# Kernel tuning notes

Measured on AMD Instinct MI355X. Metric: run time of the kernel, lower is better.

## Reference

```python
import jax, jax.numpy as jnp
import numpy as np

TEMP = 10.0  # softmax_ called with N=10.0 in reduce_func

def qmul(a, b):
    # Hamilton product, rows are (w, x, y, z)
    aw, ax, ay, az = a[..., 0], a[..., 1], a[..., 2], a[..., 3]
    bw, bx, by, bz = b[..., 0], b[..., 1], b[..., 2], b[..., 3]
    return jnp.stack([
        aw * bw - ax * bx - ay * by - az * bz,
        aw * bx + ax * bw + ay * bz - az * by,
        aw * by - ax * bz + ay * bw + az * bx,
        aw * bz + ax * by - ay * bx + az * bw,
    ], axis=-1)

def setup_inputs() -> dict:
    key = jax.random.key(0)
    k1, k2, k3, k4, k5, k6 = jax.random.split(key, 6)
    N, E = 100000, 3200000
    node_levels = jax.random.uniform(k1, (N,), dtype=jnp.float32)
    node_q = jax.random.normal(k2, (N, 4), dtype=jnp.float32)
    node_q = node_q / jnp.linalg.norm(node_q, axis=1, keepdims=True)
    edge_rel_q = jax.random.normal(k3, (E, 4), dtype=jnp.float32)
    edge_rel_q = edge_rel_q / jnp.linalg.norm(edge_rel_q, axis=1, keepdims=True)
    edge_w = jax.random.uniform(k4, (E,), dtype=jnp.float32)
    src = jax.random.randint(k5, (E,), 0, N, dtype=jnp.int32)
    dst = jax.random.randint(k6, (E,), 0, N, dtype=jnp.int32)
    return {"node_levels": node_levels, "node_q": node_q,
            "edge_rel_q": edge_rel_q, "edge_w": edge_w,
            "src": src, "dst": dst}

def reference(node_levels, node_q, edge_rel_q, edge_w, src, dst):
    N = node_q.shape[0]
    # per-edge message: accumulated quaternion rel_q * q_src
    accu_q = qmul(edge_rel_q, node_q[src])          # [E,4]
    l_src = node_levels[src]                        # [E]
    # softmax logits: cost = w * l (self term has w = 1)
    cost_e = TEMP * edge_w * l_src                  # [E]
    cost_self = TEMP * node_levels                  # [N]
    # segmented stable softmax over {self} U in-edges per dst node
    seg_max = jax.ops.segment_max(cost_e, dst, num_segments=N)
    m = jnp.maximum(seg_max, cost_self)             # [N]
    exp_e = jnp.exp(cost_e - m[dst])                # [E]
    exp_self = jnp.exp(cost_self - m)               # [N]
    Z = jax.ops.segment_sum(exp_e, dst, num_segments=N) + exp_self
    # weighted sums
    sum_q = jax.ops.segment_sum(exp_e[:, None] * accu_q, dst, num_segments=N) \
            + exp_self[:, None] * node_q            # [N,4]
    sum_l = jax.ops.segment_sum(exp_e * l_src, dst, num_segments=N) \
            + exp_self * node_levels                # [N]
    out_q = sum_q / Z[:, None]
    out_levels = sum_l / Z
    # F.normalize(q, p=2, dim=1) with eps=1e-12 clamp
    norm = jnp.maximum(jnp.linalg.norm(out_q, axis=1, keepdims=True), 1e-12)
    return out_q / norm, out_levels
```

## Files before the change

### kernel.cpp

```cpp
#include <hip/hip_runtime.h>
#include <hip/hip_fp16.h>

#define TEMP 10.0f
#define TPB 512
#define HTPB 256
#define NBLK 1024
#define SHIFT 9
#define GSZ 512
#define BMAX 256
#define TILE 1568
#define GTPB 1024
#define GT 4096

typedef float v2f  __attribute__((ext_vector_type(2)));
typedef float vf4  __attribute__((ext_vector_type(4)));
typedef unsigned uv4 __attribute__((ext_vector_type(4)));

__device__ __forceinline__ int   nt_i (const int* p)   { return __builtin_nontemporal_load(p); }
__device__ __forceinline__ float nt_f (const float* p) { return __builtin_nontemporal_load(p); }
__device__ __forceinline__ float4 nt_f4(const float4* p) {
    vf4 v = __builtin_nontemporal_load((const vf4*)p);
    return make_float4(v.x, v.y, v.z, v.w);
}
__device__ __forceinline__ uint4 nt_u4(const uint4* p) {
    uv4 v = __builtin_nontemporal_load((const uv4*)p);
    uint4 r; r.x = v.x; r.y = v.y; r.z = v.z; r.w = v.w; return r;
}

__device__ __forceinline__ void pk_fadd(float* p, float a, float b) {
#if __has_builtin(__builtin_amdgcn_global_atomic_fadd_v2f32)
    v2f v; v.x = a; v.y = b;
    __builtin_amdgcn_global_atomic_fadd_v2f32(
        (__attribute__((address_space(1))) v2f*)p, v);
#else
    atomicAdd(p, a); atomicAdd(p + 1, b);
#endif
}

__device__ __forceinline__ void hamilton(float4 a, float4 b,
                                         float& ow, float& ox, float& oy, float& oz) {
    ow = a.x*b.x - a.y*b.y - a.z*b.z - a.w*b.w;
    ox = a.x*b.y + a.y*b.x + a.z*b.w - a.w*b.z;
    oy = a.x*b.z - a.y*b.w + a.z*b.x + a.w*b.y;
    oz = a.x*b.w + a.y*b.z - a.z*b.y + a.w*b.x;
}

__device__ __forceinline__ unsigned f2h(float x) {
    return (unsigned)__half_as_ushort(__float2half_rn(x));
}
__device__ __forceinline__ float h2f(unsigned u) {
    return __half2float(__ushort_as_half((unsigned short)(u & 0xFFFFu)));
}

__global__ void __launch_bounds__(HTPB)
hist_kernel(const int* __restrict__ dst, unsigned* __restrict__ blkhist,
            int E, int B, int span) {
    extern __shared__ unsigned h[];
    for (int i = threadIdx.x; i < B; i += blockDim.x) h[i] = 0;
    __syncthreads();
    int start = blockIdx.x * span;
    int end = start + span; if (end > E) end = E;
    for (int e = start + threadIdx.x; e < end; e += blockDim.x)
        atomicAdd(&h[((unsigned)nt_i(&dst[e])) >> SHIFT], 1u);
    __syncthreads();
    for (int i = threadIdx.x; i < B; i += blockDim.x)
        blkhist[(size_t)i * gridDim.x + blockIdx.x] = h[i];
}

__global__ void __launch_bounds__(1024)
scan_blocks_kernel(unsigned* __restrict__ blkhist, unsigned* __restrict__ totals) {
    __shared__ unsigned s[1024];
    int b = blockIdx.x, t = threadIdx.x, n = blockDim.x;
    unsigned v = blkhist[(size_t)b * n + t];
    s[t] = v; __syncthreads();
    for (int off = 1; off < n; off <<= 1) {
        unsigned add = (t >= off) ? s[t - off] : 0u;
        __syncthreads();
        s[t] += add;
        __syncthreads();
    }
    blkhist[(size_t)b * n + t] = s[t] - v;
    if (t == n - 1) totals[b] = s[t];
}

__global__ void __launch_bounds__(1024)
scan_totals_kernel(const unsigned* __restrict__ totals,
                   unsigned* __restrict__ offsets, int B) {
    __shared__ unsigned s[1024];
    int t = threadIdx.x;
    unsigned v = (t < B) ? totals[t] : 0u;
    s[t] = v; __syncthreads();
    for (int off = 1; off < 1024; off <<= 1) {
        unsigned add = (t >= off) ? s[t - off] : 0u;
        __syncthreads();
        s[t] += add;
        __syncthreads();
    }
    if (t < B) offsets[t] = s[t] - v;
    if (t == B - 1) offsets[B] = s[t];
}

__global__ void __launch_bounds__(TPB)
scatter_sort_kernel(const float* __restrict__ nl, const float4* __restrict__ nq,
                    const float4* __restrict__ erq, const float* __restrict__ ew,
                    const int* __restrict__ src, const int* __restrict__ dst,
                    const unsigned* __restrict__ blkhist,
                    const unsigned* __restrict__ offsets,
                    uint4* __restrict__ buckets,
                    int E, int B, int span) {
    __shared__ uint4    stage[TILE];
    __shared__ unsigned gslot[TILE];
    __shared__ unsigned gcur[BMAX];
    __shared__ unsigned th[BMAX];
    __shared__ unsigned basec[BMAX];
    __shared__ unsigned curt[BMAX];

    int blk = blockIdx.x, nb = gridDim.x, tid = threadIdx.x;
    for (int b = tid; b < B; b += TPB)
        gcur[b] = offsets[b] + blkhist[(size_t)b * nb + blk];
    int start = blk * span;
    int end = start + span; if (end > E) end = E;

    for (int ts = start; ts < end; ts += TILE) {
        int tE = end - ts; if (tE > TILE) tE = TILE;
        for (int b = tid; b < B; b += TPB) th[b] = 0;
        __syncthreads();
        for (int k = tid; k < tE; k += TPB)
            atomicAdd(&th[((unsigned)dst[ts + k]) >> SHIFT], 1u);
        __syncthreads();
        if (tid < 64) {
            int lane = tid;
            unsigned vals[4];
            unsigned tot = 0;
            #pragma unroll
            for (int c = 0; c < 4; ++c) {
                int i = lane * 4 + c;
                vals[c] = (i < B) ? th[i] : 0u;
                tot += vals[c];
            }
            unsigned inc = tot;
            #pragma unroll
            for (int off = 1; off < 64; off <<= 1) {
                unsigned up = __shfl_up(inc, off);
                if (lane >= off) inc += up;
            }
            unsigned run = inc - tot;
            #pragma unroll
            for (int c = 0; c < 4; ++c) {
                int i = lane * 4 + c;
                if (i < B) { basec[i] = run; curt[i] = run; }
                run += vals[c];
            }
        }
        __syncthreads();
        for (int k = tid; k < tE; k += TPB) {
            int e = ts + k;
            int s_ = nt_i(&src[e]);
            unsigned d = (unsigned)dst[e];
            float l = nl[s_];
            float p = __expf(TEMP * nt_f(&ew[e]) * l);
            float ow, ox, oy, oz;
            hamilton(nt_f4(&erq[e]), nq[s_], ow, ox, oy, oz);
            unsigned b = d >> SHIFT;
            unsigned pos = atomicAdd(&curt[b], 1u);
            uint4 pk;
            pk.x = (d & (GSZ - 1)) | (f2h(p) << 16);
            pk.y = f2h(p * l)  | (f2h(p * ow) << 16);
            pk.z = f2h(p * ox) | (f2h(p * oy) << 16);
            pk.w = f2h(p * oz);
            stage[pos] = pk;
            gslot[pos] = gcur[b] + (pos - basec[b]);
        }
        __syncthreads();
        for (int k = tid; k < tE; k += TPB)
            buckets[gslot[k]] = stage[k];
        __syncthreads();
        for (int b = tid; b < B; b += TPB) gcur[b] += th[b];
        __syncthreads();
    }
}

__global__ void __launch_bounds__(GTPB)
gather_sort_kernel(const float* __restrict__ nl, const float4* __restrict__ nq,
                   const unsigned* __restrict__ offsets,
                   const uint4* __restrict__ buckets,
                   float4* __restrict__ out_q, float* __restrict__ out_l, int N) {
    __shared__ unsigned s0a[GT];
    __shared__ unsigned s1a[GT];
    __shared__ unsigned s2a[GT];
    __shared__ unsigned cnt[GSZ];
    __shared__ unsigned base[GSZ + 1];

    int b = blockIdx.x, tid = threadIdx.x;
    unsigned q0 = offsets[b], q1 = offsets[b + 1];
    int M = (int)(q1 - q0);

    float accZ = 0.f, accL = 0.f, accW = 0.f, accX = 0.f, accY = 0.f, accV = 0.f;

    for (int t0 = 0; t0 < M; t0 += GT) {
        int tGT = M - t0; if (tGT > GT) tGT = GT;
        for (int i = tid; i < GSZ; i += GTPB) cnt[i] = 0;
        __syncthreads();

        uint4 pk0, pk1, pk2, pk3;
        int i0 = tid, i1 = tid + GTPB, i2 = tid + 2 * GTPB, i3 = tid + 3 * GTPB;
        if (i0 < tGT) { pk0 = nt_u4(&buckets[q0 + t0 + i0]); atomicAdd(&cnt[pk0.x & (GSZ-1)], 1u); }
        if (i1 < tGT) { pk1 = nt_u4(&buckets[q0 + t0 + i1]); atomicAdd(&cnt[pk1.x & (GSZ-1)], 1u); }
        if (i2 < tGT) { pk2 = nt_u4(&buckets[q0 + t0 + i2]); atomicAdd(&cnt[pk2.x & (GSZ-1)], 1u); }
        if (i3 < tGT) { pk3 = nt_u4(&buckets[q0 + t0 + i3]); atomicAdd(&cnt[pk3.x & (GSZ-1)], 1u); }
        __syncthreads();

        if (tid < 64) {
            unsigned vals[8], tot = 0;
            #pragma unroll
            for (int c = 0; c < 8; ++c) { vals[c] = cnt[tid * 8 + c]; tot += vals[c]; }
            unsigned inc = tot;
            #pragma unroll
            for (int off = 1; off < 64; off <<= 1) {
                unsigned up = __shfl_up(inc, off);
                if (tid >= off) inc += up;
            }
            unsigned run = inc - tot;
            #pragma unroll
            for (int c = 0; c < 8; ++c) {
                base[tid * 8 + c] = run;
                cnt[tid * 8 + c]  = run;
                run += vals[c];
            }
            if (tid == 63) base[GSZ] = run;
        }
        __syncthreads();

        if (i0 < tGT) { unsigned p = atomicAdd(&cnt[pk0.x & (GSZ-1)], 1u);
                        s0a[p] = (pk0.x >> 16) | (pk0.w << 16); s1a[p] = pk0.y; s2a[p] = pk0.z; }
        if (i1 < tGT) { unsigned p = atomicAdd(&cnt[pk1.x & (GSZ-1)], 1u);
                        s0a[p] = (pk1.x >> 16) | (pk1.w << 16); s1a[p] = pk1.y; s2a[p] = pk1.z; }
        if (i2 < tGT) { unsigned p = atomicAdd(&cnt[pk2.x & (GSZ-1)], 1u);
                        s0a[p] = (pk2.x >> 16) | (pk2.w << 16); s1a[p] = pk2.y; s2a[p] = pk2.z; }
        if (i3 < tGT) { unsigned p = atomicAdd(&cnt[pk3.x & (GSZ-1)], 1u);
                        s0a[p] = (pk3.x >> 16) | (pk3.w << 16); s1a[p] = pk3.y; s2a[p] = pk3.z; }
        __syncthreads();

        if (tid < GSZ) {
            unsigned lo = base[tid], hi = base[tid + 1];
            for (unsigned p = lo; p < hi; ++p) {
                unsigned a = s0a[p], d = s1a[p], e = s2a[p];
                accZ += h2f(a);        accV += h2f(a >> 16);
                accL += h2f(d);        accW += h2f(d >> 16);
                accX += h2f(e);        accY += h2f(e >> 16);
            }
        }
        __syncthreads();
    }

    if (tid < GSZ) {
        int n = b * GSZ + tid;
        if (n < N) {
            float l  = nl[n];
            float ps = __expf(TEMP * l);
            float Z  = accZ + ps;
            float sl = accL + ps * l;
            float4 q = nq[n];
            float qw = accW + ps * q.x;
            float qx = accX + ps * q.y;
            float qy = accY + ps * q.z;
            float qz = accV + ps * q.w;
            float inv = 1.0f / Z;
            qw *= inv; qx *= inv; qy *= inv; qz *= inv;
            float norm = fmaxf(sqrtf(qw*qw + qx*qx + qy*qy + qz*qz), 1e-12f);
            float rn = 1.0f / norm;
            out_q[n] = make_float4(qw * rn, qx * rn, qy * rn, qz * rn);
            out_l[n] = sl * inv;
        }
    }
}

__global__ void __launch_bounds__(256)
scatter_kernel(const int* __restrict__ dst, int* __restrict__ cnt,
               int* __restrict__ bucket, int cap,
               const float* __restrict__ node_levels, const float4* __restrict__ node_q,
               const float4* __restrict__ edge_rel_q, const float* __restrict__ edge_w,
               const int* __restrict__ src, float* __restrict__ side, int E) {
    int e = blockIdx.x * blockDim.x + threadIdx.x;
    if (e >= E) return;
    int d = dst[e];
    int slot = atomicAdd(&cnt[d], 1);
    if (slot < cap) {
        bucket[(long long)d * cap + slot] = e;
    } else {
        int s = src[e];
        float l = node_levels[s];
        float p = __expf(TEMP * edge_w[e] * l);
        float ow, ox, oy, oz;
        hamilton(edge_rel_q[e], node_q[s], ow, ox, oy, oz);
        float* rec = side + 6 * (long long)d;
        pk_fadd(rec + 0, p,      p * l);
        pk_fadd(rec + 2, p * ow, p * ox);
        pk_fadd(rec + 4, p * oy, p * oz);
    }
}

__global__ void __launch_bounds__(256)
gather_kernel(const float* __restrict__ node_levels, const float4* __restrict__ node_q,
              const float4* __restrict__ edge_rel_q, const float* __restrict__ edge_w,
              const int* __restrict__ src, const int* __restrict__ cnt,
              const int* __restrict__ bucket, int cap, const float* __restrict__ side,
              float4* __restrict__ out_q, float* __restrict__ out_l, int N) {
    int tid  = blockIdx.x * blockDim.x + threadIdx.x;
    int wave = tid >> 6, lane = tid & 63, half = lane >> 5, sub = lane & 31;
    int n = wave * 2 + half;
    float aZ = 0.f, aL = 0.f, a0 = 0.f, a1 = 0.f, a2 = 0.f, a3 = 0.f;
    if (n < N) {
        int deg = cnt[n]; if (deg > cap) deg = cap;
        const int* bkt = bucket + (long long)n * cap;
        for (int s = sub; s < deg; s += 32) {
            int e = bkt[s];
            int sn = src[e];
            float l = node_levels[sn];
            float p = __expf(TEMP * edge_w[e] * l);
            float ow, ox, oy, oz;
            hamilton(edge_rel_q[e], node_q[sn], ow, ox, oy, oz);
            aZ += p; aL += p * l; a0 += p * ow; a1 += p * ox; a2 += p * oy; a3 += p * oz;
        }
    }
    for (int m = 16; m; m >>= 1) {
        aZ += __shfl_xor(aZ, m); aL += __shfl_xor(aL, m);
        a0 += __shfl_xor(a0, m); a1 += __shfl_xor(a1, m);
        a2 += __shfl_xor(a2, m); a3 += __shfl_xor(a3, m);
    }
    if (sub == 0 && n < N) {
        const float* rec = side + 6 * (long long)n;
        float l  = node_levels[n];
        float ps = __expf(TEMP * l);
        float Z  = aZ + rec[0] + ps;
        float sl = aL + rec[1] + ps * l;
        float4 q = node_q[n];
        float qw = a0 + rec[2] + ps * q.x;
        float qx = a1 + rec[3] + ps * q.y;
        float qy = a2 + rec[4] + ps * q.z;
        float qz = a3 + rec[5] + ps * q.w;
        float inv = 1.0f / Z;
        qw *= inv; qx *= inv; qy *= inv; qz *= inv;
        float norm = fmaxf(sqrtf(qw*qw + qx*qx + qy*qy + qz*qz), 1e-12f);
        float rn = 1.0f / norm;
        out_q[n] = make_float4(qw * rn, qx * rn, qy * rn, qz * rn);
        out_l[n] = sl * inv;
    }
}

extern "C" void kernel_launch(void* const* d_in, const int* in_sizes, int n_in,
                              void* d_out, int out_size, void* d_ws, size_t ws_size,
                              hipStream_t stream) {
    const float*  node_levels = (const float*)d_in[0];
    const float4* node_q      = (const float4*)d_in[1];
    const float4* edge_rel_q  = (const float4*)d_in[2];
    const float*  edge_w      = (const float*)d_in[3];
    const int*    src         = (const int*)d_in[4];
    const int*    dst         = (const int*)d_in[5];

    const int N = in_sizes[0];
    const int E = in_sizes[3];

    const int B = (N + GSZ - 1) / GSZ;
    const int span = (E + NBLK - 1) / NBLK;

    size_t head_elems   = (size_t)B * NBLK + B + (B + 1);
    size_t buckets_byte = (head_elems * 4 + 15) & ~(size_t)15;
    size_t need         = buckets_byte + (size_t)E * 16;

    if (need <= ws_size && B <= BMAX) {
        unsigned* blkhist = (unsigned*)d_ws;
        unsigned* totals  = blkhist + (size_t)B * NBLK;
        unsigned* offsets = totals + B;
        uint4*    buckets = (uint4*)((char*)d_ws + buckets_byte);

        hist_kernel<<<NBLK, HTPB, B * 4, stream>>>(dst, blkhist, E, B, span);
        scan_blocks_kernel<<<B, NBLK, 0, stream>>>(blkhist, totals);
        scan_totals_kernel<<<1, 1024, 0, stream>>>(totals, offsets, B);
        scatter_sort_kernel<<<NBLK, TPB, 0, stream>>>(
            node_levels, node_q, edge_rel_q, edge_w, src, dst,
            blkhist, offsets, buckets, E, B, span);
        gather_sort_kernel<<<B, GTPB, 0, stream>>>(
            node_levels, node_q, offsets, buckets,
            (float4*)d_out, (float*)d_out + 4 * (long long)N, N);
    } else {
        const int tpb = 256;
        size_t cnt_elems  = ((size_t)N + 3) & ~(size_t)3;
        size_t side_elems = 6 * (size_t)N;
        size_t head_bytes = (cnt_elems + side_elems) * 4;
        int cap = 0;
        for (int c : {128, 64}) {
            if (head_bytes + (size_t)N * c * 4 <= ws_size) { cap = c; break; }
        }
        int*   cnt    = (int*)d_ws;
        float* side   = (float*)d_ws + cnt_elems;
        int*   bucket = (int*)d_ws + cnt_elems + side_elems;
        hipMemsetAsync(d_ws, 0, head_bytes, stream);
        scatter_kernel<<<(E + tpb - 1) / tpb, tpb, 0, stream>>>(
            dst, cnt, bucket, cap, node_levels, node_q, edge_rel_q, edge_w, src, side, E);
        int waves  = (N + 1) / 2;
        int blocks = (waves * 64 + tpb - 1) / tpb;
        gather_kernel<<<blocks, tpb, 0, stream>>>(
            node_levels, node_q, edge_rel_q, edge_w, src, cnt, bucket, cap, side,
            (float4*)d_out, (float*)d_out + 4 * (long long)N, N);
    }
}
```

Measured before the change: 209.7 us.

## Restructure scatter tile loop to register-cache indices and batch gathers

The scatter kernel now loads dst and src once per tile into registers, with three elements per thread, instead of reading dst twice. It issues the node gathers for all three elements before the compute to raise memory-level parallelism. The gcur update moves into the scan phase on idle threads, and the histogram reset is folded into the end-of-tile barrier, which cuts the synchronisations per tile. TILE shrinks to 1536 so the tile is exactly 3x512, and launch bounds add an occupancy hint, at the cost of more registers per thread.

```diff
diff --git a/kernel.cpp b/kernel.cpp
--- a/kernel.cpp
+++ b/kernel.cpp
@@ -8,7 +8,7 @@
 #define SHIFT 9
 #define GSZ 512
 #define BMAX 256
-#define TILE 1568
+#define TILE 1536
 #define GTPB 1024
 #define GT 4096
 
@@ -100,7 +100,7 @@
     if (t == B - 1) offsets[B] = s[t];
 }
 
-__global__ void __launch_bounds__(TPB)
+__global__ void __launch_bounds__(TPB, 8)
 scatter_sort_kernel(const float* __restrict__ nl, const float4* __restrict__ nq,
                     const float4* __restrict__ erq, const float* __restrict__ ew,
                     const int* __restrict__ src, const int* __restrict__ dst,
@@ -114,20 +114,32 @@
     __shared__ unsigned th[BMAX];
     __shared__ unsigned basec[BMAX];
     __shared__ unsigned curt[BMAX];
+    __shared__ unsigned gbase[BMAX];
 
     int blk = blockIdx.x, nb = gridDim.x, tid = threadIdx.x;
-    for (int b = tid; b < B; b += TPB)
+    for (int b = tid; b < B; b += TPB) {
         gcur[b] = offsets[b] + blkhist[(size_t)b * nb + blk];
+        th[b] = 0;
+    }
     int start = blk * span;
     int end = start + span; if (end > E) end = E;
+    __syncthreads();
 
     for (int ts = start; ts < end; ts += TILE) {
         int tE = end - ts; if (tE > TILE) tE = TILE;
-        for (int b = tid; b < B; b += TPB) th[b] = 0;
-        __syncthreads();
-        for (int k = tid; k < tE; k += TPB)
-            atomicAdd(&th[((unsigned)dst[ts + k]) >> SHIFT], 1u);
-        __syncthreads();
+
+        int s_[3]; unsigned d_[3];
+        #pragma unroll
+        for (int j = 0; j < 3; ++j) {
+            int k = tid + j * TPB;
+            if (k < tE) {
+                d_[j] = (unsigned)nt_i(&dst[ts + k]);
+                s_[j] = nt_i(&src[ts + k]);
+                atomicAdd(&th[d_[j] >> SHIFT], 1u);
+            }
+        }
+        __syncthreads();
+
         if (tid < 64) {
             int lane = tid;
             unsigned vals[4];
@@ -151,31 +163,42 @@
                 if (i < B) { basec[i] = run; curt[i] = run; }
                 run += vals[c];
             }
-        }
-        __syncthreads();
-        for (int k = tid; k < tE; k += TPB) {
-            int e = ts + k;
-            int s_ = nt_i(&src[e]);
-            unsigned d = (unsigned)dst[e];
-            float l = nl[s_];
-            float p = __expf(TEMP * nt_f(&ew[e]) * l);
-            float ow, ox, oy, oz;
-            hamilton(nt_f4(&erq[e]), nq[s_], ow, ox, oy, oz);
-            unsigned b = d >> SHIFT;
-            unsigned pos = atomicAdd(&curt[b], 1u);
-            uint4 pk;
-            pk.x = (d & (GSZ - 1)) | (f2h(p) << 16);
-            pk.y = f2h(p * l)  | (f2h(p * ow) << 16);
-            pk.z = f2h(p * ox) | (f2h(p * oy) << 16);
-            pk.w = f2h(p * oz);
-            stage[pos] = pk;
-            gslot[pos] = gcur[b] + (pos - basec[b]);
-        }
-        __syncthreads();
+        } else if (tid >= 256) {
+            for (int b = tid - 256; b < B; b += TPB - 256) {
+                gbase[b] = gcur[b];
+                gcur[b] += th[b];
+            }
+        }
+        __syncthreads();
+
+        float l_[3]; float4 q_[3];
+        #pragma unroll
+        for (int j = 0; j < 3; ++j) { int k = tid + j * TPB; if (k < tE) l_[j] = nl[s_[j]]; }
+        #pragma unroll
+        for (int j = 0; j < 3; ++j) { int k = tid + j * TPB; if (k < tE) q_[j] = nq[s_[j]]; }
+        #pragma unroll
+        for (int j = 0; j < 3; ++j) {
+            int k = tid + j * TPB;
+            if (k < tE) {
+                float p = __expf(TEMP * nt_f(&ew[ts + k]) * l_[j]);
+                float ow, ox, oy, oz;
+                hamilton(nt_f4(&erq[ts + k]), q_[j], ow, ox, oy, oz);
+                unsigned b = d_[j] >> SHIFT;
+                unsigned pos = atomicAdd(&curt[b], 1u);
+                uint4 pk;
+                pk.x = (d_[j] & (GSZ - 1)) | (f2h(p) << 16);
+                pk.y = f2h(p * l_[j]) | (f2h(p * ow) << 16);
+                pk.z = f2h(p * ox) | (f2h(p * oy) << 16);
+                pk.w = f2h(p * oz);
+                stage[pos] = pk;
+                gslot[pos] = gbase[b] + (pos - basec[b]);
+            }
+        }
+        __syncthreads();
+
         for (int k = tid; k < tE; k += TPB)
             buckets[gslot[k]] = stage[k];
-        __syncthreads();
-        for (int b = tid; b < B; b += TPB) gcur[b] += th[b];
+        for (int b = tid; b < B; b += TPB) th[b] = 0;
         __syncthreads();
     }
 }
```

After: 206.9 us. About the same (-1.4%).

## Pack node data into one float4, scatter directly to buckets, split gather accumulation

Applied to the files above, without the earlier changes.

Adds a pre-pass that packs each node's level and quaternion into a single float4, storing the level's magnitude with w's sign and rebuilding w from the unit-norm constraint, so each edge needs one gathered 16-byte load instead of two. The scatter kernel drops the per-tile shared-memory staging and local sort and writes each packed edge record straight to its global bucket slot via a shared atomic cursor. This gives up coalescing of the bucket writes in exchange for removing two barriers per tile and the shared-memory footprint, which allows more resident blocks. The gather kernel now uses two threads per node and combines them with a lane shuffle, so all 1024 threads take part in the reduction. Reconstructing w via sqrt adds some rounding error.

```diff
diff --git a/kernel.cpp b/kernel.cpp
--- a/kernel.cpp
+++ b/kernel.cpp
@@ -8,7 +8,6 @@
 #define SHIFT 9
 #define GSZ 512
 #define BMAX 256
-#define TILE 1568
 #define GTPB 1024
 #define GT 4096
 
@@ -50,6 +49,16 @@
 }
 __device__ __forceinline__ float h2f(unsigned u) {
     return __half2float(__ushort_as_half((unsigned short)(u & 0xFFFFu)));
+}
+
+__global__ void __launch_bounds__(256)
+pack_kernel(const float* __restrict__ nl, const float4* __restrict__ nq,
+            float4* __restrict__ pack, int N) {
+    int n = blockIdx.x * 256 + threadIdx.x;
+    if (n >= N) return;
+    float l = nl[n];
+    float4 q = nq[n];
+    pack[n] = make_float4(copysignf(l, q.w), q.x, q.y, q.z);
 }
 
 __global__ void __launch_bounds__(HTPB)
@@ -100,83 +109,41 @@
     if (t == B - 1) offsets[B] = s[t];
 }
 
-__global__ void __launch_bounds__(TPB)
-scatter_sort_kernel(const float* __restrict__ nl, const float4* __restrict__ nq,
-                    const float4* __restrict__ erq, const float* __restrict__ ew,
-                    const int* __restrict__ src, const int* __restrict__ dst,
-                    const unsigned* __restrict__ blkhist,
-                    const unsigned* __restrict__ offsets,
-                    uint4* __restrict__ buckets,
-                    int E, int B, int span) {
-    __shared__ uint4    stage[TILE];
-    __shared__ unsigned gslot[TILE];
+__global__ void __launch_bounds__(TPB, 8)
+scatter_direct_kernel(const float4* __restrict__ pack,
+                      const float4* __restrict__ erq, const float* __restrict__ ew,
+                      const int* __restrict__ src, const int* __restrict__ dst,
+                      const unsigned* __restrict__ blkhist,
+                      const unsigned* __restrict__ offsets,
+                      uint4* __restrict__ buckets,
+                      int E, int B, int span) {
     __shared__ unsigned gcur[BMAX];
-    __shared__ unsigned th[BMAX];
-    __shared__ unsigned basec[BMAX];
-    __shared__ unsigned curt[BMAX];
-
     int blk = blockIdx.x, nb = gridDim.x, tid = threadIdx.x;
     for (int b = tid; b < B; b += TPB)
         gcur[b] = offsets[b] + blkhist[(size_t)b * nb + blk];
+    __syncthreads();
     int start = blk * span;
     int end = start + span; if (end > E) end = E;
 
-    for (int ts = start; ts < end; ts += TILE) {
-        int tE = end - ts; if (tE > TILE) tE = TILE;
-        for (int b = tid; b < B; b += TPB) th[b] = 0;
-        __syncthreads();
-        for (int k = tid; k < tE; k += TPB)
-            atomicAdd(&th[((unsigned)dst[ts + k]) >> SHIFT], 1u);
-        __syncthreads();
-        if (tid < 64) {
-            int lane = tid;
-            unsigned vals[4];
-            unsigned tot = 0;
-            #pragma unroll
-            for (int c = 0; c < 4; ++c) {
-                int i = lane * 4 + c;
-                vals[c] = (i < B) ? th[i] : 0u;
-                tot += vals[c];
-            }
-            unsigned inc = tot;
-            #pragma unroll
-            for (int off = 1; off < 64; off <<= 1) {
-                unsigned up = __shfl_up(inc, off);
-                if (lane >= off) inc += up;
-            }
-            unsigned run = inc - tot;
-            #pragma unroll
-            for (int c = 0; c < 4; ++c) {
-                int i = lane * 4 + c;
-                if (i < B) { basec[i] = run; curt[i] = run; }
-                run += vals[c];
-            }
-        }
-        __syncthreads();
-        for (int k = tid; k < tE; k += TPB) {
-            int e = ts + k;
-            int s_ = nt_i(&src[e]);
-            unsigned d = (unsigned)dst[e];
-            float l = nl[s_];
-            float p = __expf(TEMP * nt_f(&ew[e]) * l);
-            float ow, ox, oy, oz;
-            hamilton(nt_f4(&erq[e]), nq[s_], ow, ox, oy, oz);
-            unsigned b = d >> SHIFT;
-            unsigned pos = atomicAdd(&curt[b], 1u);
-            uint4 pk;
-            pk.x = (d & (GSZ - 1)) | (f2h(p) << 16);
-            pk.y = f2h(p * l)  | (f2h(p * ow) << 16);
-            pk.z = f2h(p * ox) | (f2h(p * oy) << 16);
-            pk.w = f2h(p * oz);
-            stage[pos] = pk;
-            gslot[pos] = gcur[b] + (pos - basec[b]);
-        }
-        __syncthreads();
-        for (int k = tid; k < tE; k += TPB)
-            buckets[gslot[k]] = stage[k];
-        __syncthreads();
-        for (int b = tid; b < B; b += TPB) gcur[b] += th[b];
-        __syncthreads();
+    #pragma unroll 2
+    for (int e = start + tid; e < end; e += TPB) {
+        int s_ = nt_i(&src[e]);
+        unsigned d = (unsigned)nt_i(&dst[e]);
+        float4 pq = pack[s_];
+        float l  = fabsf(pq.x);
+        float qw = pq.y, qx = pq.z, qy = pq.w;
+        float qz = copysignf(sqrtf(fmaxf(0.f, 1.f - qw*qw - qx*qx - qy*qy)), pq.x);
+        float p = __expf(TEMP * nt_f(&ew[e]) * l);
+        float ow, ox, oy, oz;
+        hamilton(nt_f4(&erq[e]), make_float4(qw, qx, qy, qz), ow, ox, oy, oz);
+        unsigned b = d >> SHIFT;
+        unsigned slot = atomicAdd(&gcur[b], 1u);
+        uint4 pk;
+        pk.x = (d & (GSZ - 1)) | (f2h(p) << 16);
+        pk.y = f2h(p * l) | (f2h(p * ow) << 16);
+        pk.z = f2h(p * ox) | (f2h(p * oy) << 16);
+        pk.w = f2h(p * oz);
+        buckets[slot] = pk;
     }
 }
 
@@ -241,9 +208,10 @@
                         s0a[p] = (pk3.x >> 16) | (pk3.w << 16); s1a[p] = pk3.y; s2a[p] = pk3.z; }
         __syncthreads();
 
-        if (tid < GSZ) {
-            unsigned lo = base[tid], hi = base[tid + 1];
-            for (unsigned p = lo; p < hi; ++p) {
+        {
+            int j = tid >> 1, r = tid & 1;
+            unsigned lo = base[j], hi = base[j + 1];
+            for (unsigned p = lo + r; p < hi; p += 2) {
                 unsigned a = s0a[p], d = s1a[p], e = s2a[p];
                 accZ += h2f(a);        accV += h2f(a >> 16);
                 accL += h2f(d);        accW += h2f(d >> 16);
@@ -253,8 +221,12 @@
         __syncthreads();
     }
 
-    if (tid < GSZ) {
-        int n = b * GSZ + tid;
+    accZ += __shfl_xor(accZ, 1); accL += __shfl_xor(accL, 1);
+    accW += __shfl_xor(accW, 1); accX += __shfl_xor(accX, 1);
+    accY += __shfl_xor(accY, 1); accV += __shfl_xor(accV, 1);
+    if ((tid & 1) == 0) {
+        int j = tid >> 1;
+        int n = b * GSZ + j;
         if (n < N) {
             float l  = nl[n];
             float ps = __expf(TEMP * l);
@@ -366,19 +338,23 @@
 
     size_t head_elems   = (size_t)B * NBLK + B + (B + 1);
     size_t buckets_byte = (head_elems * 4 + 15) & ~(size_t)15;
-    size_t need         = buckets_byte + (size_t)E * 16;
+    size_t pack_byte    = buckets_byte + (size_t)E * 16;
+    size_t need         = pack_byte + (size_t)N * 16;
 
     if (need <= ws_size && B <= BMAX) {
         unsigned* blkhist = (unsigned*)d_ws;
         unsigned* totals  = blkhist + (size_t)B * NBLK;
         unsigned* offsets = totals + B;
         uint4*    buckets = (uint4*)((char*)d_ws + buckets_byte);
-
+        float4*   pack    = (float4*)((char*)d_ws + pack_byte);
+
+        pack_kernel<<<(N + 255) / 256, 256, 0, stream>>>(
+            node_levels, node_q, pack, N);
         hist_kernel<<<NBLK, HTPB, B * 4, stream>>>(dst, blkhist, E, B, span);
         scan_blocks_kernel<<<B, NBLK, 0, stream>>>(blkhist, totals);
         scan_totals_kernel<<<1, 1024, 0, stream>>>(totals, offsets, B);
-        scatter_sort_kernel<<<NBLK, TPB, 0, stream>>>(
-            node_levels, node_q, edge_rel_q, edge_w, src, dst,
+        scatter_direct_kernel<<<NBLK, TPB, 0, stream>>>(
+            pack, edge_rel_q, edge_w, src, dst,
             blkhist, offsets, buckets, E, B, span);
         gather_sort_kernel<<<B, GTPB, 0, stream>>>(
             node_levels, node_q, offsets, buckets,
```

Result: slower. 219.6 us (+4.7%).
